# Kernel tuning notes

Hardware: AMD Instinct MI355X
Metric: run time of the kernel (lower is better)

The kernel has to match this reference:

```python
import jax, jax.numpy as jnp
import numpy as np

N_SEND = 12288   # 12 * 32^2
N_REC = 49152    # 12 * 64^2
E = 196608       # 4 * N_REC (knn with k=4)
D = 256
EIN, EOUT = 4, 256
LIN_IN, LIN_OUT = 512, 256
B = 2


def setup_inputs() -> dict:
    key = jax.random.key(0)
    ks = jax.random.split(key, 12)
    s = 0.05
    x = jax.random.normal(ks[0], (B, N_SEND, D), jnp.float32)
    edge_attr = jax.random.normal(ks[1], (E, EIN), jnp.float32)
    idx_send = jax.random.randint(ks[2], (E,), 0, N_SEND, dtype=jnp.int32)
    idx_rec = jnp.sort(jax.random.randint(ks[3], (E,), 0, N_REC, dtype=jnp.int32))
    return {
        "x": x,
        "edge_attr": edge_attr,
        "idx_send": idx_send,
        "idx_rec": idx_rec,
        "We1": jax.random.normal(ks[4], (EIN, EOUT), jnp.float32) * s,
        "be1": jnp.zeros((EOUT,), jnp.float32),
        "We2": jax.random.normal(ks[5], (EOUT, EOUT), jnp.float32) * s,
        "be2": jnp.zeros((EOUT,), jnp.float32),
        "Wl1": jax.random.normal(ks[6], (LIN_IN, LIN_OUT), jnp.float32) * s,
        "bl1": jnp.zeros((LIN_OUT,), jnp.float32),
        "Wl2": jax.random.normal(ks[7], (LIN_OUT, LIN_OUT), jnp.float32) * s,
        "bl2": jnp.zeros((LIN_OUT,), jnp.float32),
    }


def reference(x, edge_attr, idx_send, idx_rec, We1, be1, We2, be2, Wl1, bl1, Wl2, bl2):
    # edge embedder MLP: Linear -> GELU -> Linear   [E, EOUT]
    ef = jax.nn.gelu(edge_attr @ We1 + be1) @ We2 + be2
    # gather sender node features by edge           [B, E, D]
    v_s = x[:, idx_send, :]
    # concat gathered features with (batch-broadcast) edge embeddings [B, E, D+EOUT]
    ef_b = jnp.broadcast_to(ef[None], (v_s.shape[0],) + ef.shape)
    v_s_prime = jnp.concatenate([v_s, ef_b], axis=-1)
    # scatter_sum over receiver index along edge dim -> [B, N_REC, LIN_IN]
    agg = jax.vmap(lambda m: jax.ops.segment_sum(m, idx_rec, num_segments=N_REC))(v_s_prime)
    # final FeedForward: Linear -> GELU -> Linear
    return jax.nn.gelu(agg @ Wl1 + bl1) @ Wl2 + bl2
```

## Files before the change

### kernel.cpp

```cpp
#include <hip/hip_runtime.h>
#include <hip/hip_bf16.h>

#define N_SEND 12288
#define N_REC  49152
#define NEDGE  196608
#define RECV   16

typedef __attribute__((ext_vector_type(8)))  short short8;
typedef __attribute__((ext_vector_type(4)))  short shortx4;
typedef __attribute__((ext_vector_type(4)))  float floatx4;
typedef __attribute__((ext_vector_type(16))) float floatx16;
typedef __attribute__((ext_vector_type(4)))  unsigned int uintx4;

__device__ inline short f2bs(float f) {
    __hip_bfloat16 h = __float2bfloat16(f);
    return *reinterpret_cast<short*>(&h);
}
__device__ inline float gelu_tanh(float x) {
    const float k0 = 0.7978845608028654f;
    float u = k0 * (x + 0.044715f * x * x * x);
    float e = __expf(2.0f * u);
    float t = 1.0f - 2.0f / (e + 1.0f);
    return 0.5f * x * (1.0f + t);
}

__global__ void prep_kernel(const float* __restrict__ We2, const float* __restrict__ be2,
                            const float* __restrict__ Wl1, const float* __restrict__ Wl2,
                            short* __restrict__ BT1, short* __restrict__ WT2,
                            float* __restrict__ cvec) {
    int i = blockIdx.x;
    int n = threadIdx.x;
    if (i < 256) {
        float acc = 0.f;
        for (int j = 0; j < 256; ++j)
            acc += We2[i * 256 + j] * Wl1[(256 + j) * 256 + n];
        BT1[n * 512 + i]       = f2bs(Wl1[i * 256 + n]);
        BT1[n * 512 + 256 + i] = f2bs(acc);
        WT2[n * 256 + i]       = f2bs(Wl2[i * 256 + n]);
    } else {
        float acc = 0.f;
        for (int j = 0; j < 256; ++j)
            acc += be2[j] * Wl1[(256 + j) * 256 + n];
        cvec[n] = acc;
    }
}

__global__ void xcast_kernel(const float* __restrict__ X, short* __restrict__ Xb) {
    int i = (blockIdx.x * 256 + threadIdx.x) * 8;
    int row = i >> 8;
    int c   = i & 255;
    int bb_ = (row >= N_SEND) ? 1 : 0;
    int n   = row - bb_ * N_SEND;
    floatx4 v0 = *(const floatx4*)(X + i);
    floatx4 v1 = *(const floatx4*)(X + i + 4);
    short8 p;
#pragma unroll
    for (int j = 0; j < 4; ++j) { p[j] = f2bs(v0[j]); p[j + 4] = f2bs(v1[j]); }
    *(short8*)(Xb + (size_t)n * 512 + bb_ * 256 + c) = p;
}

__global__ void bounds_kernel(const int* __restrict__ idx_rec, int* __restrict__ bnd) {
    int r = blockIdx.x * 256 + threadIdx.x;
    if (r > N_REC) return;
    int lo = 0, hi = NEDGE;
    while (lo < hi) { int mid = (lo + hi) >> 1; if (idx_rec[mid] < r) lo = mid + 1; else hi = mid; }
    bnd[r] = lo;
}

#define XTU(f, row) ((((f) * 32) + ((row) ^ ((f) & 7))) * 8)
#define HTU(f, rl)  ((((f) * 16) + ((rl) ^ ((f) & 7))) * 8)

__global__ __launch_bounds__(512, 8)
void fused16(const int* __restrict__ idx_send, const int* __restrict__ bnd,
             const float* __restrict__ EA, const float* __restrict__ We1,
             const float* __restrict__ be1, const short* __restrict__ Xb,
             const short* __restrict__ BT1, const short* __restrict__ WT2,
             const float* __restrict__ cvec, const float* __restrict__ bl1,
             const float* __restrict__ bl2, float* __restrict__ OUT) {
    __shared__ __attribute__((aligned(16))) short XT[32 * 32 * 8];
    __shared__ __attribute__((aligned(16))) short HT[32 * 16 * 8];
    __shared__ int sb[RECV + 1];

    int t = threadIdx.x;
    int r0 = blockIdx.x * RECV;
    if (t <= RECV) sb[t] = bnd[r0 + t];
    __syncthreads();

    {
        int cg = t & 31;
        int b  = (t >> 5) & 1;
        int rh = t >> 6;
        int c8 = cg * 8;
        int hc = c8 + 4 * b;

        floatx4 w0 = *(const floatx4*)(We1 + hc);
        floatx4 w1 = *(const floatx4*)(We1 + 256 + hc);
        floatx4 w2 = *(const floatx4*)(We1 + 512 + hc);
        floatx4 w3 = *(const floatx4*)(We1 + 768 + hc);
        floatx4 bb = *(const floatx4*)(be1 + hc);
        const short* xb_t = Xb + b * 256 + c8;

#pragma unroll
        for (int r = 0; r < 2; ++r) {
            int rl = rh * 2 + r;
            int es = __builtin_amdgcn_readfirstlane(sb[rl]);
            int ee = __builtin_amdgcn_readfirstlane(sb[rl + 1]);

            float xacc[8];
            float hacc[4];
#pragma unroll
            for (int c = 0; c < 8; ++c) xacc[c] = 0.f;
#pragma unroll
            for (int c = 0; c < 4; ++c) hacc[c] = 0.f;

            int s = 0; floatx4 a = {0.f, 0.f, 0.f, 0.f};
            if (es < ee) { s = idx_send[es]; a = *(const floatx4*)(EA + (size_t)es * 4); }
            for (int e = es; e < ee; ++e) {
                int cs = s; floatx4 ca = a;
                int ep = (e + 1 < ee) ? e + 1 : e;
                s = idx_send[ep];
                a = *(const floatx4*)(EA + (size_t)ep * 4);
                uintx4 xv = *(const uintx4*)(xb_t + (size_t)cs * 512);
#pragma unroll
                for (int dw = 0; dw < 4; ++dw) {
                    xacc[2 * dw]     += __builtin_bit_cast(float, xv[dw] << 16);
                    xacc[2 * dw + 1] += __builtin_bit_cast(float, xv[dw] & 0xffff0000u);
                }
#pragma unroll
                for (int j = 0; j < 4; ++j) {
                    float u = ca[0] * w0[j] + ca[1] * w1[j] + ca[2] * w2[j] + ca[3] * w3[j] + bb[j];
                    hacc[j] += gelu_tanh(u);
                }
            }
            short8 xp;
#pragma unroll
            for (int c = 0; c < 8; ++c) xp[c] = f2bs(xacc[c]);
            *(short8*)(XT + XTU(cg, b * RECV + rl)) = xp;
            shortx4 hp;
#pragma unroll
            for (int c = 0; c < 4; ++c) hp[c] = f2bs(hacc[c]);
            *(shortx4*)(HT + HTU(cg, rl) + 4 * b) = hp;
        }
    }
    __syncthreads();

    int w = t >> 6, lane = t & 63;
    int m = lane & 31, q = lane >> 5;
    int wcol = w * 32;
    floatx16 acc;
#pragma unroll
    for (int j = 0; j < 16; ++j) acc[j] = 0.f;

    const short* Bp1 = BT1 + (size_t)(wcol + m) * 512 + q * 8;
#pragma unroll
    for (int ci = 0; ci < 8; ++ci) {
#pragma unroll
        for (int kk = 0; kk < 4; ++kk) {
            short8 bv = *(const short8*)(Bp1 + ci * 64 + kk * 16);
            int f = ci * 8 + 2 * kk + q;
            short8 a0;
            if (ci < 4) {
                a0 = *(const short8*)(XT + XTU(f, m));
            } else {
                a0 = *(const short8*)(HT + HTU(f - 32, m & 15));
            }
            acc = __builtin_amdgcn_mfma_f32_32x32x16_bf16(bv, a0, acc, 0, 0, 0);
        }
    }
    __syncthreads();

    {
        int rl = m & 15;
        float cntv = (float)(sb[rl + 1] - sb[rl]);
#pragma unroll
        for (int qd = 0; qd < 4; ++qd) {
            int c0 = wcol + qd * 8 + q * 4;
            floatx4 cv  = *(const floatx4*)(cvec + c0);
            floatx4 b1v = *(const floatx4*)(bl1 + c0);
            shortx4 pk;
#pragma unroll
            for (int j = 0; j < 4; ++j)
                pk[j] = f2bs(gelu_tanh(acc[qd * 4 + j] + cntv * cv[j] + b1v[j]));
            *(shortx4*)(XT + XTU(w * 4 + qd, m) + q * 4) = pk;
        }
#pragma unroll
        for (int j = 0; j < 16; ++j) acc[j] = 0.f;
    }
    __syncthreads();

    const short* Bp2 = WT2 + (size_t)(wcol + m) * 256 + q * 8;
#pragma unroll
    for (int ci = 0; ci < 4; ++ci) {
#pragma unroll
        for (int kk = 0; kk < 4; ++kk) {
            short8 bv = *(const short8*)(Bp2 + ci * 64 + kk * 16);
            int f2 = ci * 8 + 2 * kk + q;
            short8 a0 = *(const short8*)(XT + XTU(f2, m));
            acc = __builtin_amdgcn_mfma_f32_32x32x16_bf16(bv, a0, acc, 0, 0, 0);
        }
    }

    {
        int bat = m >> 4;
        int rl = m & 15;
        size_t obase = ((size_t)bat * N_REC + r0 + rl) * 256;
#pragma unroll
        for (int qd = 0; qd < 4; ++qd) {
            int c0 = wcol + qd * 8 + q * 4;
            floatx4 bv = *(const floatx4*)(bl2 + c0);
            floatx4 o;
#pragma unroll
            for (int j = 0; j < 4; ++j)
                o[j] = acc[qd * 4 + j] + bv[j];
            *(floatx4*)(OUT + obase + c0) = o;
        }
    }
}

extern "C" void kernel_launch(void* const* d_in, const int* in_sizes, int n_in,
                              void* d_out, int out_size, void* d_ws, size_t ws_size,
                              hipStream_t stream) {
    const float* x        = (const float*)d_in[0];
    const float* ea       = (const float*)d_in[1];
    const int*   idx_send = (const int*)d_in[2];
    const int*   idx_rec  = (const int*)d_in[3];
    const float* We1      = (const float*)d_in[4];
    const float* be1      = (const float*)d_in[5];
    const float* We2      = (const float*)d_in[6];
    const float* be2      = (const float*)d_in[7];
    const float* Wl1      = (const float*)d_in[8];
    const float* bl1      = (const float*)d_in[9];
    const float* Wl2      = (const float*)d_in[10];
    const float* bl2      = (const float*)d_in[11];
    float* out = (float*)d_out;
    char*  ws  = (char*)d_ws;

    short* BT1  = (short*)(ws + 0);
    short* WT2  = (short*)(ws + 262144);
    float* cvec = (float*)(ws + 393216);
    int*   bnd  = (int*)  (ws + 397312);
    short* Xb   = (short*)(ws + 1048576);

    prep_kernel<<<257, 256, 0, stream>>>(We2, be2, Wl1, Wl2, BT1, WT2, cvec);
    xcast_kernel<<<(2 * N_SEND * 256) / (256 * 8), 256, 0, stream>>>(x, Xb);
    bounds_kernel<<<(N_REC + 1 + 255) / 256, 256, 0, stream>>>(idx_rec, bnd);
    fused16<<<N_REC / RECV, 512, 0, stream>>>(idx_send, bnd, ea, We1, be1, Xb,
                                              BT1, WT2, cvec, bl1, bl2, out);
}
```

Before: 331.9 us.

## Stage gathered sender rows into LDS via async global_load_lds chunks

The per-thread serial edge loop, where each thread loaded its own gathered sender row, is replaced by a block-cooperative scheme. Each chunk of 32 edges first has its sender indices and edge attributes staged in shared memory. The whole wavefront set then issues direct global-to-LDS 16-byte loads of the bf16 sender rows and computes the GELU edge-embedding sums while those copies are in flight, so the dependent gather latency is overlapped with compute and issued with more parallelism. The cost is a 32 KB LDS buffer, extra barriers per chunk, and fewer resident blocks (launch bounds lowered from 8 to 4).

```diff
diff --git a/kernel.cpp b/kernel.cpp
--- a/kernel.cpp
+++ b/kernel.cpp
@@ -5,6 +5,7 @@
 #define N_REC  49152
 #define NEDGE  196608
 #define RECV   16
+#define CHK    32
 
 typedef __attribute__((ext_vector_type(8)))  short short8;
 typedef __attribute__((ext_vector_type(4)))  short shortx4;
@@ -22,6 +23,12 @@
     float e = __expf(2.0f * u);
     float t = 1.0f - 2.0f / (e + 1.0f);
     return 0.5f * x * (1.0f + t);
+}
+
+__device__ inline void gload_lds16(const short* g, short* l) {
+    __builtin_amdgcn_global_load_lds(
+        (const __attribute__((address_space(1))) unsigned int*)g,
+        (__attribute__((address_space(3))) unsigned int*)l, 16, 0, 0);
 }
 
 __global__ void prep_kernel(const float* __restrict__ We2, const float* __restrict__ be2,
@@ -70,81 +77,115 @@
 #define XTU(f, row) ((((f) * 32) + ((row) ^ ((f) & 7))) * 8)
 #define HTU(f, rl)  ((((f) * 16) + ((rl) ^ ((f) & 7))) * 8)
 
-__global__ __launch_bounds__(512, 8)
+__global__ __launch_bounds__(512, 4)
 void fused16(const int* __restrict__ idx_send, const int* __restrict__ bnd,
              const float* __restrict__ EA, const float* __restrict__ We1,
              const float* __restrict__ be1, const short* __restrict__ Xb,
              const short* __restrict__ BT1, const short* __restrict__ WT2,
              const float* __restrict__ cvec, const float* __restrict__ bl1,
              const float* __restrict__ bl2, float* __restrict__ OUT) {
+    __shared__ __attribute__((aligned(16))) short SBUF[CHK * 512];
     __shared__ __attribute__((aligned(16))) short XT[32 * 32 * 8];
     __shared__ __attribute__((aligned(16))) short HT[32 * 16 * 8];
-    __shared__ int sb[RECV + 1];
+    __shared__ int   sb[RECV + 1];
+    __shared__ int   s_idx[CHK];
+    __shared__ __attribute__((aligned(16))) float s_ea[CHK * 4];
 
     int t = threadIdx.x;
     int r0 = blockIdx.x * RECV;
     if (t <= RECV) sb[t] = bnd[r0 + t];
     __syncthreads();
+    int e0 = sb[0], eN = sb[RECV];
+
+    int cg = t & 31;
+    int b  = (t >> 5) & 1;
+    int rh = t >> 6;
+    int lane = t & 63;
+    int c8 = cg * 8;
+    int hc = c8 + 4 * b;
 
     {
-        int cg = t & 31;
-        int b  = (t >> 5) & 1;
-        int rh = t >> 6;
-        int c8 = cg * 8;
-        int hc = c8 + 4 * b;
-
         floatx4 w0 = *(const floatx4*)(We1 + hc);
         floatx4 w1 = *(const floatx4*)(We1 + 256 + hc);
         floatx4 w2 = *(const floatx4*)(We1 + 512 + hc);
         floatx4 w3 = *(const floatx4*)(We1 + 768 + hc);
         floatx4 bb = *(const floatx4*)(be1 + hc);
-        const short* xb_t = Xb + b * 256 + c8;
-
+
+        float xacc[2][8];
+        float hacc[2][4];
+#pragma unroll
+        for (int r = 0; r < 2; ++r) {
+#pragma unroll
+            for (int c = 0; c < 8; ++c) xacc[r][c] = 0.f;
+#pragma unroll
+            for (int c = 0; c < 4; ++c) hacc[r][c] = 0.f;
+        }
+
+        for (int base = e0; base < eN; base += CHK) {
+            int cnt = min(CHK, eN - base);
+            __syncthreads();
+            if (t < cnt) {
+                s_idx[t] = idx_send[base + t];
+                *(floatx4*)(s_ea + 4 * t) = *(const floatx4*)(EA + (size_t)(base + t) * 4);
+            }
+            __syncthreads();
+#pragma unroll
+            for (int k = 0; k < 4; ++k) {
+                int slot = rh + 8 * k;
+                if (slot < cnt) {
+                    int s = s_idx[slot];
+                    gload_lds16(Xb + (size_t)s * 512 + lane * 8,
+                                SBUF + slot * 512 + lane * 8);
+                }
+            }
+#pragma unroll
+            for (int r = 0; r < 2; ++r) {
+                int rl = rh * 2 + r;
+                int es = max(sb[rl], base);
+                int ee = min(sb[rl + 1], base + cnt);
+                for (int e = es; e < ee; ++e) {
+                    floatx4 a = *(const floatx4*)(s_ea + 4 * (e - base));
+#pragma unroll
+                    for (int j = 0; j < 4; ++j) {
+                        float u = a[0] * w0[j] + a[1] * w1[j] + a[2] * w2[j]
+                                + a[3] * w3[j] + bb[j];
+                        hacc[r][j] += gelu_tanh(u);
+                    }
+                }
+            }
+            __syncthreads();
+#pragma unroll
+            for (int r = 0; r < 2; ++r) {
+                int rl = rh * 2 + r;
+                int es = max(sb[rl], base);
+                int ee = min(sb[rl + 1], base + cnt);
+                for (int e = es; e < ee; ++e) {
+                    int li = e - base;
+                    uintx4 xv = *(const uintx4*)(SBUF + li * 512 + b * 256 + c8);
+#pragma unroll
+                    for (int dw = 0; dw < 4; ++dw) {
+                        xacc[r][2 * dw]     += __builtin_bit_cast(float, xv[dw] << 16);
+                        xacc[r][2 * dw + 1] += __builtin_bit_cast(float, xv[dw] & 0xffff0000u);
+                    }
+                }
+            }
+        }
 #pragma unroll
         for (int r = 0; r < 2; ++r) {
             int rl = rh * 2 + r;
-            int es = __builtin_amdgcn_readfirstlane(sb[rl]);
-            int ee = __builtin_amdgcn_readfirstlane(sb[rl + 1]);
-
-            float xacc[8];
-            float hacc[4];
-#pragma unroll
-            for (int c = 0; c < 8; ++c) xacc[c] = 0.f;
-#pragma unroll
-            for (int c = 0; c < 4; ++c) hacc[c] = 0.f;
-
-            int s = 0; floatx4 a = {0.f, 0.f, 0.f, 0.f};
-            if (es < ee) { s = idx_send[es]; a = *(const floatx4*)(EA + (size_t)es * 4); }
-            for (int e = es; e < ee; ++e) {
-                int cs = s; floatx4 ca = a;
-                int ep = (e + 1 < ee) ? e + 1 : e;
-                s = idx_send[ep];
-                a = *(const floatx4*)(EA + (size_t)ep * 4);
-                uintx4 xv = *(const uintx4*)(xb_t + (size_t)cs * 512);
-#pragma unroll
-                for (int dw = 0; dw < 4; ++dw) {
-                    xacc[2 * dw]     += __builtin_bit_cast(float, xv[dw] << 16);
-                    xacc[2 * dw + 1] += __builtin_bit_cast(float, xv[dw] & 0xffff0000u);
-                }
-#pragma unroll
-                for (int j = 0; j < 4; ++j) {
-                    float u = ca[0] * w0[j] + ca[1] * w1[j] + ca[2] * w2[j] + ca[3] * w3[j] + bb[j];
-                    hacc[j] += gelu_tanh(u);
-                }
-            }
             short8 xp;
 #pragma unroll
-            for (int c = 0; c < 8; ++c) xp[c] = f2bs(xacc[c]);
+            for (int c = 0; c < 8; ++c) xp[c] = f2bs(xacc[r][c]);
             *(short8*)(XT + XTU(cg, b * RECV + rl)) = xp;
             shortx4 hp;
 #pragma unroll
-            for (int c = 0; c < 4; ++c) hp[c] = f2bs(hacc[c]);
+            for (int c = 0; c < 4; ++c) hp[c] = f2bs(hacc[r][c]);
             *(shortx4*)(HT + HTU(cg, rl) + 4 * b) = hp;
         }
     }
     __syncthreads();
 
-    int w = t >> 6, lane = t & 63;
+    int w = t >> 6;
     int m = lane & 31, q = lane >> 5;
     int wcol = w * 32;
     floatx16 acc;
```

Result: slower. 370.2 us (+11.6%).

## Halve block to 256 threads, two MFMA column tiles per wave, prefetch gather

Applied to the files above, without the earlier changes.

The fused kernel now runs with 4 waves instead of 8 per block. Each wave handles 4 receivers in the gather phase and two 32-column output tiles in both GEMMs, so each A fragment read from LDS feeds two MFMAs. The gather loop now prefetches the next edge's bf16 node row as well as its index and edge attributes, giving more loads in flight. The cost is more registers per thread (two accumulators, launch bounds 256,5), which may reduce occupancy, and fewer waves to hide gather latency.

```diff
diff --git a/kernel.cpp b/kernel.cpp
--- a/kernel.cpp
+++ b/kernel.cpp
@@ -70,13 +70,13 @@
 #define XTU(f, row) ((((f) * 32) + ((row) ^ ((f) & 7))) * 8)
 #define HTU(f, rl)  ((((f) * 16) + ((rl) ^ ((f) & 7))) * 8)
 
-__global__ __launch_bounds__(512, 8)
-void fused16(const int* __restrict__ idx_send, const int* __restrict__ bnd,
-             const float* __restrict__ EA, const float* __restrict__ We1,
-             const float* __restrict__ be1, const short* __restrict__ Xb,
-             const short* __restrict__ BT1, const short* __restrict__ WT2,
-             const float* __restrict__ cvec, const float* __restrict__ bl1,
-             const float* __restrict__ bl2, float* __restrict__ OUT) {
+__global__ __launch_bounds__(256, 5)
+void fused16b(const int* __restrict__ idx_send, const int* __restrict__ bnd,
+              const float* __restrict__ EA, const float* __restrict__ We1,
+              const float* __restrict__ be1, const short* __restrict__ Xb,
+              const short* __restrict__ BT1, const short* __restrict__ WT2,
+              const float* __restrict__ cvec, const float* __restrict__ bl1,
+              const float* __restrict__ bl2, float* __restrict__ OUT) {
     __shared__ __attribute__((aligned(16))) short XT[32 * 32 * 8];
     __shared__ __attribute__((aligned(16))) short HT[32 * 16 * 8];
     __shared__ int sb[RECV + 1];
@@ -86,10 +86,12 @@
     if (t <= RECV) sb[t] = bnd[r0 + t];
     __syncthreads();
 
+    int lane = t & 63;
+    int w = t >> 6;
+
     {
-        int cg = t & 31;
-        int b  = (t >> 5) & 1;
-        int rh = t >> 6;
+        int cg = lane & 31;
+        int b  = lane >> 5;
         int c8 = cg * 8;
         int hc = c8 + 4 * b;
 
@@ -101,8 +103,8 @@
         const short* xb_t = Xb + b * 256 + c8;
 
 #pragma unroll
-        for (int r = 0; r < 2; ++r) {
-            int rl = rh * 2 + r;
+        for (int r = 0; r < 4; ++r) {
+            int rl = w * 4 + r;
             int es = __builtin_amdgcn_readfirstlane(sb[rl]);
             int ee = __builtin_amdgcn_readfirstlane(sb[rl + 1]);
 
@@ -113,23 +115,27 @@
 #pragma unroll
             for (int c = 0; c < 4; ++c) hacc[c] = 0.f;
 
-            int s = 0; floatx4 a = {0.f, 0.f, 0.f, 0.f};
-            if (es < ee) { s = idx_send[es]; a = *(const floatx4*)(EA + (size_t)es * 4); }
-            for (int e = es; e < ee; ++e) {
-                int cs = s; floatx4 ca = a;
-                int ep = (e + 1 < ee) ? e + 1 : e;
-                s = idx_send[ep];
-                a = *(const floatx4*)(EA + (size_t)ep * 4);
-                uintx4 xv = *(const uintx4*)(xb_t + (size_t)cs * 512);
-#pragma unroll
-                for (int dw = 0; dw < 4; ++dw) {
-                    xacc[2 * dw]     += __builtin_bit_cast(float, xv[dw] << 16);
-                    xacc[2 * dw + 1] += __builtin_bit_cast(float, xv[dw] & 0xffff0000u);
-                }
-#pragma unroll
-                for (int j = 0; j < 4; ++j) {
-                    float u = ca[0] * w0[j] + ca[1] * w1[j] + ca[2] * w2[j] + ca[3] * w3[j] + bb[j];
-                    hacc[j] += gelu_tanh(u);
+            if (es < ee) {
+                int     sC  = idx_send[es];
+                floatx4 aC  = *(const floatx4*)(EA + (size_t)es * 4);
+                uintx4  xvC = *(const uintx4*)(xb_t + (size_t)sC * 512);
+                for (int e = es; e < ee; ++e) {
+                    int ep = (e + 1 < ee) ? e + 1 : e;
+                    int     sN  = idx_send[ep];
+                    floatx4 aN  = *(const floatx4*)(EA + (size_t)ep * 4);
+                    uintx4  xvN = *(const uintx4*)(xb_t + (size_t)sN * 512);
+#pragma unroll
+                    for (int dw = 0; dw < 4; ++dw) {
+                        xacc[2 * dw]     += __builtin_bit_cast(float, xvC[dw] << 16);
+                        xacc[2 * dw + 1] += __builtin_bit_cast(float, xvC[dw] & 0xffff0000u);
+                    }
+#pragma unroll
+                    for (int j = 0; j < 4; ++j) {
+                        float u = aC[0] * w0[j] + aC[1] * w1[j] + aC[2] * w2[j]
+                                + aC[3] * w3[j] + bb[j];
+                        hacc[j] += gelu_tanh(u);
+                    }
+                    sC = sN; aC = aN; xvC = xvN;
                 }
             }
             short8 xp;
@@ -144,19 +150,19 @@
     }
     __syncthreads();
 
-    int w = t >> 6, lane = t & 63;
     int m = lane & 31, q = lane >> 5;
-    int wcol = w * 32;
-    floatx16 acc;
-#pragma unroll
-    for (int j = 0; j < 16; ++j) acc[j] = 0.f;
-
-    const short* Bp1 = BT1 + (size_t)(wcol + m) * 512 + q * 8;
+    floatx16 acc0, acc1;
+#pragma unroll
+    for (int j = 0; j < 16; ++j) { acc0[j] = 0.f; acc1[j] = 0.f; }
+
+    const short* Bp1a = BT1 + (size_t)(w * 64 + m) * 512 + q * 8;
+    const short* Bp1b = BT1 + (size_t)(w * 64 + 32 + m) * 512 + q * 8;
 #pragma unroll
     for (int ci = 0; ci < 8; ++ci) {
 #pragma unroll
         for (int kk = 0; kk < 4; ++kk) {
-            short8 bv = *(const short8*)(Bp1 + ci * 64 + kk * 16);
+            short8 bva = *(const short8*)(Bp1a + ci * 64 + kk * 16);
+            short8 bvb = *(const short8*)(Bp1b + ci * 64 + kk * 16);
             int f = ci * 8 + 2 * kk + q;
             short8 a0;
             if (ci < 4) {
@@ -164,7 +170,8 @@
             } else {
                 a0 = *(const short8*)(HT + HTU(f - 32, m & 15));
             }
-            acc = __builtin_amdgcn_mfma_f32_32x32x16_bf16(bv, a0, acc, 0, 0, 0);
+            acc0 = __builtin_amdgcn_mfma_f32_32x32x16_bf16(bva, a0, acc0, 0, 0, 0);
+            acc1 = __builtin_amdgcn_mfma_f32_32x32x16_bf16(bvb, a0, acc1, 0, 0, 0);
         }
     }
     __syncthreads();
@@ -173,30 +180,37 @@
         int rl = m & 15;
         float cntv = (float)(sb[rl + 1] - sb[rl]);
 #pragma unroll
-        for (int qd = 0; qd < 4; ++qd) {
-            int c0 = wcol + qd * 8 + q * 4;
-            floatx4 cv  = *(const floatx4*)(cvec + c0);
-            floatx4 b1v = *(const floatx4*)(bl1 + c0);
-            shortx4 pk;
-#pragma unroll
-            for (int j = 0; j < 4; ++j)
-                pk[j] = f2bs(gelu_tanh(acc[qd * 4 + j] + cntv * cv[j] + b1v[j]));
-            *(shortx4*)(XT + XTU(w * 4 + qd, m) + q * 4) = pk;
-        }
-#pragma unroll
-        for (int j = 0; j < 16; ++j) acc[j] = 0.f;
-    }
-    __syncthreads();
-
-    const short* Bp2 = WT2 + (size_t)(wcol + m) * 256 + q * 8;
+        for (int ct = 0; ct < 2; ++ct) {
+            const floatx16& ac = ct ? acc1 : acc0;
+#pragma unroll
+            for (int qd = 0; qd < 4; ++qd) {
+                int c0 = w * 64 + ct * 32 + qd * 8 + q * 4;
+                floatx4 cv  = *(const floatx4*)(cvec + c0);
+                floatx4 b1v = *(const floatx4*)(bl1 + c0);
+                shortx4 pk;
+#pragma unroll
+                for (int j = 0; j < 4; ++j)
+                    pk[j] = f2bs(gelu_tanh(ac[qd * 4 + j] + cntv * cv[j] + b1v[j]));
+                *(shortx4*)(XT + XTU(w * 8 + ct * 4 + qd, m) + q * 4) = pk;
+            }
+        }
+#pragma unroll
+        for (int j = 0; j < 16; ++j) { acc0[j] = 0.f; acc1[j] = 0.f; }
+    }
+    __syncthreads();
+
+    const short* Bp2a = WT2 + (size_t)(w * 64 + m) * 256 + q * 8;
+    const short* Bp2b = WT2 + (size_t)(w * 64 + 32 + m) * 256 + q * 8;
 #pragma unroll
     for (int ci = 0; ci < 4; ++ci) {
 #pragma unroll
         for (int kk = 0; kk < 4; ++kk) {
-            short8 bv = *(const short8*)(Bp2 + ci * 64 + kk * 16);
+            short8 bva = *(const short8*)(Bp2a + ci * 64 + kk * 16);
+            short8 bvb = *(const short8*)(Bp2b + ci * 64 + kk * 16);
             int f2 = ci * 8 + 2 * kk + q;
             short8 a0 = *(const short8*)(XT + XTU(f2, m));
-            acc = __builtin_amdgcn_mfma_f32_32x32x16_bf16(bv, a0, acc, 0, 0, 0);
+            acc0 = __builtin_amdgcn_mfma_f32_32x32x16_bf16(bva, a0, acc0, 0, 0, 0);
+            acc1 = __builtin_amdgcn_mfma_f32_32x32x16_bf16(bvb, a0, acc1, 0, 0, 0);
         }
     }
 
@@ -205,14 +219,18 @@
         int rl = m & 15;
         size_t obase = ((size_t)bat * N_REC + r0 + rl) * 256;
 #pragma unroll
-        for (int qd = 0; qd < 4; ++qd) {
-            int c0 = wcol + qd * 8 + q * 4;
-            floatx4 bv = *(const floatx4*)(bl2 + c0);
-            floatx4 o;
-#pragma unroll
-            for (int j = 0; j < 4; ++j)
-                o[j] = acc[qd * 4 + j] + bv[j];
-            *(floatx4*)(OUT + obase + c0) = o;
+        for (int ct = 0; ct < 2; ++ct) {
+            const floatx16& ac = ct ? acc1 : acc0;
+#pragma unroll
+            for (int qd = 0; qd < 4; ++qd) {
+                int c0 = w * 64 + ct * 32 + qd * 8 + q * 4;
+                floatx4 bv = *(const floatx4*)(bl2 + c0);
+                floatx4 o;
+#pragma unroll
+                for (int j = 0; j < 4; ++j)
+                    o[j] = ac[qd * 4 + j] + bv[j];
+                *(floatx4*)(OUT + obase + c0) = o;
+            }
         }
     }
 }
@@ -244,6 +262,6 @@
     prep_kernel<<<257, 256, 0, stream>>>(We2, be2, Wl1, Wl2, BT1, WT2, cvec);
     xcast_kernel<<<(2 * N_SEND * 256) / (256 * 8), 256, 0, stream>>>(x, Xb);
     bounds_kernel<<<(N_REC + 1 + 255) / 256, 256, 0, stream>>>(idx_rec, bnd);
-    fused16<<<N_REC / RECV, 512, 0, stream>>>(idx_send, bnd, ea, We1, be1, Xb,
-                                              BT1, WT2, cvec, bl1, bl2, out);
-}
+    fused16b<<<N_REC / RECV, 256, 0, stream>>>(idx_send, bnd, ea, We1, be1, Xb,
+                                               BT1, WT2, cvec, bl1, bl2, out);
+}
```

After: 332.9 us. Within noise of the previous version (+0.3%).
